# Optimization experiments

Measured on AMD Instinct MI355X. Metric: run time of the kernel, lower is better.

The kernel has to match this reference:

```python
import jax, jax.numpy as jnp
import numpy as np

N_ATOMS = 200_000
N_PAIRS = 20_000_000
N_SPECIES = 4
N_EDGES = 101  # -> 100 bins
R_MAX_GEN = 6.5  # generate some distances beyond the last edge (they are dropped)


def setup_inputs() -> dict:
    key = jax.random.key(0)
    k1, k2, k3, k4 = jax.random.split(key, 4)
    pair_dist = jax.random.uniform(k1, (N_PAIRS,), dtype=jnp.float32) * R_MAX_GEN
    pair_first = jax.random.randint(k2, (N_PAIRS,), 0, N_ATOMS)
    pair_second = jax.random.randint(k3, (N_PAIRS,), 0, N_ATOMS)
    # strict one-hot species encoding per atom (matches hippynn's one_hot input)
    species = jax.random.randint(k4, (N_ATOMS,), 0, N_SPECIES)
    one_hot = species[:, None] == jnp.arange(N_SPECIES)[None, :]
    bins = jnp.linspace(0.0, 6.0, N_EDGES).astype(jnp.float32)  # buffer from __init__
    return {
        "pair_dist": pair_dist,
        "pair_first": pair_first,
        "pair_second": pair_second,
        "one_hot": one_hot,
        "n_molecules": 512,
        "bins": bins,
    }


def reference(pair_dist, pair_first, pair_second, one_hot, n_molecules, bins):
    # Original: for each species pair (i,j), mask pairs where one_hot[pair_first,i]
    # and one_hot[pair_second,j], then histogram masked distances into `bins` via
    # broadcast-compare + diff of counts:  count in bin b = #(bins[b] <= d < bins[b+1]).
    # Fused single-pass equivalent: bucketize each pair distance and scatter-add
    # into a flat (species_i, species_j, bin) histogram.
    n_species = one_hot.shape[-1]
    n_bins = bins.shape[0] - 1

    species = jnp.argmax(one_hot, axis=-1)          # [n_atoms], one-hot -> label
    si = species[pair_first]                        # [n_pairs]
    sj = species[pair_second]                       # [n_pairs]

    # searchsorted(side='right') - 1 gives b s.t. bins[b] <= d < bins[b+1]
    b = jnp.searchsorted(bins, pair_dist, side="right") - 1
    valid = (b >= 0) & (b < n_bins)                 # drop d < bins[0] or d >= bins[-1]
    b_safe = jnp.clip(b, 0, n_bins - 1)

    flat_idx = (si * n_species + sj) * n_bins + b_safe
    weights = valid.astype(pair_dist.dtype)
    rdf = jnp.zeros((n_species * n_species * n_bins,), dtype=pair_dist.dtype)
    rdf = rdf.at[flat_idx].add(weights)
    rdf = rdf.reshape(n_species, n_species, n_bins)
    return (rdf / n_molecules)[None]                # [1, S, S, n_bins]
```

## Files before the change

kernel.cpp:

```cpp
#include <hip/hip_runtime.h>
#include <stdint.h>


#define NSPEC 4

__device__ inline int esize_from_nzw(unsigned int nzw) {
    if (nzw >= 640) return 1;
    if (nzw >= 192) return 4;
    return 8;
}

__device__ inline int get_species(const uint8_t* oh, int atom, int E) {
    if (E == 1) {
        uint32_t v = *(const uint32_t*)(oh + (size_t)atom * 4);
        if (v & 0x000000FFu) return 0;
        if (v & 0x0000FF00u) return 1;
        if (v & 0x00FF0000u) return 2;
        return 3;
    }
    const uint8_t* p = oh + (size_t)atom * 4 * E;
    for (int s = 0; s < NSPEC; ++s) {
        bool nzb = false;
        for (int b = 0; b < E; ++b) nzb |= (p[s * E + b] != 0);
        if (nzb) return s;
    }
    return 0;
}

__global__ void k_species(const uint8_t* __restrict__ oh, int n_atoms,
                          uint32_t* __restrict__ sp2,
                          unsigned int* __restrict__ counts, int n_counts) {
    __shared__ unsigned int s_nz;
    if (threadIdx.x == 0) s_nz = 0;
    __syncthreads();
    unsigned int local = 0;
    #pragma unroll
    for (int k = 0; k < 4; ++k) {
        uint32_t v = ((const uint32_t*)oh)[threadIdx.x * 4 + k];
        local += (v != 0u);
    }
    for (int off = 32; off > 0; off >>= 1) local += __shfl_down(local, off);
    if ((threadIdx.x & 63) == 0) atomicAdd(&s_nz, local);
    __syncthreads();
    const int E = esize_from_nzw(s_nz);

    const int gid = blockIdx.x * blockDim.x + threadIdx.x;
    const int gsz = gridDim.x * blockDim.x;
    for (int j = gid; j < n_counts; j += gsz) counts[j] = 0u;

    const int nw = (n_atoms + 15) >> 4;
    for (int w = gid; w < nw; w += gsz) {
        uint32_t word = 0;
        int base = w << 4;
        int lim = n_atoms - base;
        lim = lim < 16 ? lim : 16;
        for (int k = 0; k < lim; ++k)
            word |= (uint32_t)get_species(oh, base + k, E) << (k * 2);
        sp2[w] = word;
    }
}

__launch_bounds__(1024, 8) __global__
void k_hist_lds(const float* __restrict__ dist, const int* __restrict__ pf,
                const int* __restrict__ ps, const uint32_t* __restrict__ sp2,
                const float* __restrict__ bins, int n_edges, int n_words,
                int npairs, unsigned int* __restrict__ counts) {
    extern __shared__ float2 smem2[];
    const int n_bins = n_edges - 1;
    const int nh = NSPEC * NSPEC * n_bins;
    float2* eb = smem2;
    uint32_t* tab = (uint32_t*)(eb + n_bins);
    int* h = (int*)(tab + n_words);
    __shared__ int s_uniform;

    const int tid = threadIdx.x;
    if (tid == 0) s_uniform = 1;
    __syncthreads();

    for (int j = tid; j < n_words; j += blockDim.x) tab[j] = sp2[j];
    for (int j = tid; j < nh + 8; j += blockDim.x) h[j] = 0;
    const float lo = bins[0];
    const float hi = bins[n_edges - 1];
    const float w = (hi - lo) / (float)n_bins;
    for (int j = tid; j < n_bins; j += blockDim.x) {
        float2 e = make_float2(bins[j], bins[j + 1]);
        eb[j] = e;
        float id0 = lo + (float)j * w;
        float id1 = lo + (float)(j + 1) * w;
        if (fabsf(e.x - id0) > 0.25f * w || fabsf(e.y - id1) > 0.25f * w)
            atomicAnd(&s_uniform, 0);
    }
    __syncthreads();

    const float scale = (float)n_bins / (hi - lo);
    const int gid = blockIdx.x * blockDim.x + tid;
    const int gsz = gridDim.x * blockDim.x;
    const int nquads = npairs >> 2;
    const int dump = nh + (tid & 7);

    if (s_uniform) {
        for (int q = gid; q < nquads; q += gsz) {
            float4 d4 = ((const float4*)dist)[q];
            int4 f4 = ((const int4*)pf)[q];
            int4 s4 = ((const int4*)ps)[q];
            float d[4] = {d4.x, d4.y, d4.z, d4.w};
            int a0[4] = {f4.x, f4.y, f4.z, f4.w};
            int a1[4] = {s4.x, s4.y, s4.z, s4.w};
            int g[4], vld[4];
            #pragma unroll
            for (int k = 0; k < 4; ++k) {
                int gi = (int)((d[k] - lo) * scale);
                gi = gi < n_bins - 1 ? gi : n_bins - 1;
                g[k] = gi > 0 ? gi : 0;
                vld[k] = (d[k] >= lo) & (d[k] < hi);
            }
            float2 e[4];
            uint32_t wi[4], wj[4];
            #pragma unroll
            for (int k = 0; k < 4; ++k) e[k] = eb[g[k]];
            #pragma unroll
            for (int k = 0; k < 4; ++k) {
                wi[k] = tab[(unsigned)a0[k] >> 4];
                wj[k] = tab[(unsigned)a1[k] >> 4];
            }
            #pragma unroll
            for (int k = 0; k < 4; ++k) {
                int b = g[k] - (d[k] < e[k].x) + (d[k] >= e[k].y);
                int si = (int)((wi[k] >> ((a0[k] & 15) << 1)) & 3u);
                int sj = (int)((wj[k] >> ((a1[k] & 15) << 1)) & 3u);
                int idx = (si * NSPEC + sj) * n_bins + b;
                atomicAdd(&h[vld[k] ? idx : dump], 1);
            }
        }
    } else {
        for (int q = gid; q < nquads; q += gsz) {
            float4 d4 = ((const float4*)dist)[q];
            int4 f4 = ((const int4*)pf)[q];
            int4 s4 = ((const int4*)ps)[q];
            float d[4] = {d4.x, d4.y, d4.z, d4.w};
            int a0[4] = {f4.x, f4.y, f4.z, f4.w};
            int a1[4] = {s4.x, s4.y, s4.z, s4.w};
            #pragma unroll
            for (int k = 0; k < 4; ++k) {
                if (d[k] >= lo && d[k] < hi) {
                    int b = (int)((d[k] - lo) * scale);
                    b = b < n_bins - 1 ? b : n_bins - 1;
                    b = b > 0 ? b : 0;
                    while (d[k] < eb[b].x) --b;
                    while (d[k] >= eb[b].y) ++b;
                    int si = get_species((const uint8_t*)0, 0, 0);
                    (void)si;
                    int s_i = (int)((tab[(unsigned)a0[k] >> 4] >>
                                     ((a0[k] & 15) << 1)) & 3u);
                    int s_j = (int)((tab[(unsigned)a1[k] >> 4] >>
                                     ((a1[k] & 15) << 1)) & 3u);
                    atomicAdd(&h[(s_i * NSPEC + s_j) * n_bins + b], 1);
                }
            }
        }
    }
    int tail = npairs & 3;
    if (gid < tail) {
        int i = (nquads << 2) + gid;
        float d = dist[i];
        if (d >= lo && d < hi) {
            int b = (int)((d - lo) * scale);
            b = b < n_bins - 1 ? b : n_bins - 1;
            b = b > 0 ? b : 0;
            while (d < eb[b].x) --b;
            while (d >= eb[b].y) ++b;
            int a0 = pf[i], a1 = ps[i];
            int s_i = (int)((tab[(unsigned)a0 >> 4] >> ((a0 & 15) << 1)) & 3u);
            int s_j = (int)((tab[(unsigned)a1 >> 4] >> ((a1 & 15) << 1)) & 3u);
            atomicAdd(&h[(s_i * NSPEC + s_j) * n_bins + b], 1);
        }
    }

    __syncthreads();
    for (int j = tid; j < nh; j += blockDim.x) {
        int v = h[j];
        if (v) atomicAdd(&counts[j], (unsigned int)v);
    }
}

__launch_bounds__(256, 8) __global__
void k_hist_glb(const float* __restrict__ dist, const int* __restrict__ pf,
                const int* __restrict__ ps, const uint32_t* __restrict__ sp2,
                const float* __restrict__ bins, int n_edges, int npairs,
                unsigned int* __restrict__ counts) {
    const int n_bins = n_edges - 1;
    const int nh = NSPEC * NSPEC * n_bins;
    extern __shared__ float smem[];
    float* sb = smem;
    int* h = (int*)(smem + n_edges);
    const int tid = threadIdx.x;
    for (int j = tid; j < n_edges; j += blockDim.x) sb[j] = bins[j];
    for (int j = tid; j < nh; j += blockDim.x) h[j] = 0;
    __syncthreads();
    const float lo = sb[0];
    const float hi = sb[n_edges - 1];
    const float scale = (float)n_bins / (hi - lo);
    const int gid = blockIdx.x * blockDim.x + tid;
    const int gsz = gridDim.x * blockDim.x;
    auto species_of = [&](int a) -> int {
        return (int)((sp2[a >> 4] >> ((a & 15) << 1)) & 3u);
    };
    auto bin_and_add = [&](float d, int si, int sj) {
        if (d >= lo && d < hi) {
            int b = (int)((d - lo) * scale);
            b = b < n_bins - 1 ? b : n_bins - 1;
            b = b > 0 ? b : 0;
            while (d < sb[b]) --b;
            while (d >= sb[b + 1]) ++b;
            atomicAdd(&h[(si * NSPEC + sj) * n_bins + b], 1);
        }
    };
    const int nquads = npairs >> 2;
    for (int q = gid; q < nquads; q += gsz) {
        float4 d4 = ((const float4*)dist)[q];
        int4 f4 = ((const int4*)pf)[q];
        int4 s4 = ((const int4*)ps)[q];
        bin_and_add(d4.x, species_of(f4.x), species_of(s4.x));
        bin_and_add(d4.y, species_of(f4.y), species_of(s4.y));
        bin_and_add(d4.z, species_of(f4.z), species_of(s4.z));
        bin_and_add(d4.w, species_of(f4.w), species_of(s4.w));
    }
    int tail = npairs & 3;
    if (gid < tail) {
        int i = (nquads << 2) + gid;
        bin_and_add(dist[i], species_of(pf[i]), species_of(ps[i]));
    }
    __syncthreads();
    for (int j = tid; j < nh; j += blockDim.x) {
        int v = h[j];
        if (v) atomicAdd(&counts[j], (unsigned int)v);
    }
}

__global__ void k_final(const unsigned int* __restrict__ counts,
                        const int* __restrict__ nmol, float* __restrict__ out,
                        int n) {
    int i = blockIdx.x * blockDim.x + threadIdx.x;
    if (i < n) out[i] = (float)counts[i] / (float)(*nmol);
}

extern "C" void kernel_launch(void* const* d_in, const int* in_sizes, int n_in,
                              void* d_out, int out_size, void* d_ws,
                              size_t ws_size, hipStream_t stream) {
    const float* dist = (const float*)d_in[0];
    const int* pf = (const int*)d_in[1];
    const int* ps = (const int*)d_in[2];
    const uint8_t* oh = (const uint8_t*)d_in[3];
    const int* nmol = (const int*)d_in[4];
    const float* bins = (const float*)d_in[5];
    float* out = (float*)d_out;

    const int npairs = in_sizes[0];
    const int n_edges = in_sizes[5];
    const int n_bins = n_edges - 1;
    const int n_atoms = in_sizes[3] / NSPEC;
    const int nh = NSPEC * NSPEC * n_bins;

    uint8_t* ws = (uint8_t*)d_ws;
    unsigned int* counts = (unsigned int*)ws;
    uint32_t* sp2 = (uint32_t*)(ws + nh * 4 + 64);
    const int n_words = (n_atoms + 15) >> 4;

    k_species<<<256, 256, 0, stream>>>(oh, n_atoms, sp2, counts, nh);

    const size_t shmem_lds = (size_t)n_bins * 8 + (size_t)n_words * 4 +
                             (size_t)(nh + 8) * 4;
    if (shmem_lds <= 64 * 1024) {
        k_hist_lds<<<512, 1024, shmem_lds, stream>>>(
            dist, pf, ps, sp2, bins, n_edges, n_words, npairs, counts);
    } else {
        const size_t shmem = (size_t)n_edges * 4 + (size_t)nh * 4;
        k_hist_glb<<<2048, 256, shmem, stream>>>(dist, pf, ps, sp2, bins,
                                                 n_edges, npairs, counts);
    }

    k_final<<<(out_size + 255) / 256, 256, 0, stream>>>(counts, nmol, out,
                                                        out_size);
}
```

Before: 79.71 us.

## Use contiguous per-block chunks, register prefetch, and two-way privatized LDS histograms

Each block now processes a contiguous chunk of pair quads instead of a grid-strided range, and the next iteration's float4/int4 loads are issued into registers before the current quad is binned, overlapping memory latency with LDS work. The per-block histogram is split into two copies selected by wavefront parity, which is meant to reduce LDS atomic contention, and the copies are summed at flush. The cost is extra LDS (about 6.5KB more), a larger zeroing loop, and higher register pressure from the prefetch buffers. The LDS footprint stays under the 64KB threshold, so the fast path is still taken.

Measured after the change: 82.00 us. 1.03x slower.

```diff
diff --git a/kernel.cpp b/kernel.cpp
--- a/kernel.cpp
+++ b/kernel.cpp
@@ -78,7 +78,7 @@
     __syncthreads();
 
     for (int j = tid; j < n_words; j += blockDim.x) tab[j] = sp2[j];
-    for (int j = tid; j < nh + 8; j += blockDim.x) h[j] = 0;
+    for (int j = tid; j < 2 * (nh + 8); j += blockDim.x) h[j] = 0;
     const float lo = bins[0];
     const float hi = bins[n_edges - 1];
     const float w = (hi - lo) / (float)n_bins;
@@ -93,26 +93,45 @@
     __syncthreads();
 
     const float scale = (float)n_bins / (hi - lo);
-    const int gid = blockIdx.x * blockDim.x + tid;
-    const int gsz = gridDim.x * blockDim.x;
     const int nquads = npairs >> 2;
+    const int chunk = (nquads + gridDim.x - 1) / gridDim.x;
+    const int q0 = blockIdx.x * chunk;
+    const int qend = min(q0 + chunk, nquads);
+    const int qn = qend - q0;
+    const int nit = qn > 0 ? (qn + (int)blockDim.x - 1) / (int)blockDim.x : 0;
+    int* hw = h + ((tid >> 6) & 1) * (nh + 8);
     const int dump = nh + (tid & 7);
 
-    if (s_uniform) {
-        for (int q = gid; q < nquads; q += gsz) {
-            float4 d4 = ((const float4*)dist)[q];
-            int4 f4 = ((const int4*)pf)[q];
-            int4 s4 = ((const int4*)ps)[q];
-            float d[4] = {d4.x, d4.y, d4.z, d4.w};
-            int a0[4] = {f4.x, f4.y, f4.z, f4.w};
-            int a1[4] = {s4.x, s4.y, s4.z, s4.w};
+    const float4* dist4 = (const float4*)dist;
+    const int4* pf4 = (const int4*)pf;
+    const int4* ps4 = (const int4*)ps;
+
+    if (s_uniform && nit > 0) {
+        int idx = q0 + tid;
+        int lidx = min(idx, nquads - 1);
+        float4 dA = dist4[lidx];
+        int4 fA = pf4[lidx];
+        int4 sA = ps4[lidx];
+        for (int it = 0; it < nit; ++it) {
+            float4 dB;
+            int4 fB, sB;
+            if (it + 1 < nit) {
+                int nidx = min(idx + (int)blockDim.x, nquads - 1);
+                dB = dist4[nidx];
+                fB = pf4[nidx];
+                sB = ps4[nidx];
+            }
+            const int ok = idx < qend;
+            float d[4] = {dA.x, dA.y, dA.z, dA.w};
+            int a0[4] = {fA.x, fA.y, fA.z, fA.w};
+            int a1[4] = {sA.x, sA.y, sA.z, sA.w};
             int g[4], vld[4];
             #pragma unroll
             for (int k = 0; k < 4; ++k) {
                 int gi = (int)((d[k] - lo) * scale);
                 gi = gi < n_bins - 1 ? gi : n_bins - 1;
                 g[k] = gi > 0 ? gi : 0;
-                vld[k] = (d[k] >= lo) & (d[k] < hi);
+                vld[k] = ((d[k] >= lo) & (d[k] < hi)) & ok;
             }
             float2 e[4];
             uint32_t wi[4], wj[4];
@@ -128,15 +147,19 @@
                 int b = g[k] - (d[k] < e[k].x) + (d[k] >= e[k].y);
                 int si = (int)((wi[k] >> ((a0[k] & 15) << 1)) & 3u);
                 int sj = (int)((wj[k] >> ((a1[k] & 15) << 1)) & 3u);
-                int idx = (si * NSPEC + sj) * n_bins + b;
-                atomicAdd(&h[vld[k] ? idx : dump], 1);
-            }
+                int hidx = (si * NSPEC + sj) * n_bins + b;
+                atomicAdd(&hw[vld[k] ? hidx : dump], 1);
+            }
+            dA = dB;
+            fA = fB;
+            sA = sB;
+            idx += (int)blockDim.x;
         }
-    } else {
-        for (int q = gid; q < nquads; q += gsz) {
-            float4 d4 = ((const float4*)dist)[q];
-            int4 f4 = ((const int4*)pf)[q];
-            int4 s4 = ((const int4*)ps)[q];
+    } else if (nit > 0) {
+        for (int idx = q0 + tid; idx < qend; idx += (int)blockDim.x) {
+            float4 d4 = dist4[idx];
+            int4 f4 = pf4[idx];
+            int4 s4 = ps4[idx];
             float d[4] = {d4.x, d4.y, d4.z, d4.w};
             int a0[4] = {f4.x, f4.y, f4.z, f4.w};
             int a1[4] = {s4.x, s4.y, s4.z, s4.w};
@@ -148,20 +171,19 @@
                     b = b > 0 ? b : 0;
                     while (d[k] < eb[b].x) --b;
                     while (d[k] >= eb[b].y) ++b;
-                    int si = get_species((const uint8_t*)0, 0, 0);
-                    (void)si;
                     int s_i = (int)((tab[(unsigned)a0[k] >> 4] >>
                                      ((a0[k] & 15) << 1)) & 3u);
                     int s_j = (int)((tab[(unsigned)a1[k] >> 4] >>
                                      ((a1[k] & 15) << 1)) & 3u);
-                    atomicAdd(&h[(s_i * NSPEC + s_j) * n_bins + b], 1);
+                    atomicAdd(&hw[(s_i * NSPEC + s_j) * n_bins + b], 1);
                 }
             }
         }
     }
     int tail = npairs & 3;
-    if (gid < tail) {
-        int i = (nquads << 2) + gid;
+    int gtid = blockIdx.x * (int)blockDim.x + tid;
+    if (gtid < tail) {
+        int i = (nquads << 2) + gtid;
         float d = dist[i];
         if (d >= lo && d < hi) {
             int b = (int)((d - lo) * scale);
@@ -172,13 +194,13 @@
             int a0 = pf[i], a1 = ps[i];
             int s_i = (int)((tab[(unsigned)a0 >> 4] >> ((a0 & 15) << 1)) & 3u);
             int s_j = (int)((tab[(unsigned)a1 >> 4] >> ((a1 & 15) << 1)) & 3u);
-            atomicAdd(&h[(s_i * NSPEC + s_j) * n_bins + b], 1);
+            atomicAdd(&hw[(s_i * NSPEC + s_j) * n_bins + b], 1);
         }
     }
 
     __syncthreads();
     for (int j = tid; j < nh; j += blockDim.x) {
-        int v = h[j];
+        int v = h[j] + h[nh + 8 + j];
         if (v) atomicAdd(&counts[j], (unsigned int)v);
     }
 }
@@ -269,7 +291,7 @@
     k_species<<<256, 256, 0, stream>>>(oh, n_atoms, sp2, counts, nh);
 
     const size_t shmem_lds = (size_t)n_bins * 8 + (size_t)n_words * 4 +
-                             (size_t)(nh + 8) * 4;
+                             (size_t)2 * (nh + 8) * 4;
     if (shmem_lds <= 64 * 1024) {
         k_hist_lds<<<512, 1024, shmem_lds, stream>>>(
             dist, pf, ps, sp2, bins, n_edges, n_words, npairs, counts);
```

## Verify exact fast bin index at setup and replace global atomics with per-block partial reduce

Applied to the files above, without the earlier changes.

At setup, each block checks whether the scaled-index formula maps every bin edge, and the float just below it, to the correct bin. If it does, the hot loop drops the edge-table lookup and correction step. Each block also writes its LDS histogram to a per-block partial buffer, and a new reduce kernel sums those partials and normalises, replacing the global atomicAdd merge and the final kernel. This trades contended global atomics for extra workspace traffic of HIST_BLOCKS*nh words, and falls back to the old atomic path when the workspace is too small.

New measurement: 89.47 us. 12.2% more time.

```diff
diff --git a/kernel.cpp b/kernel.cpp
--- a/kernel.cpp
+++ b/kernel.cpp
@@ -3,6 +3,7 @@
 
 
 #define NSPEC 4
+#define HIST_BLOCKS 512
 
 __device__ inline int esize_from_nzw(unsigned int nzw) {
     if (nzw >= 640) return 1;
@@ -64,60 +65,69 @@
 void k_hist_lds(const float* __restrict__ dist, const int* __restrict__ pf,
                 const int* __restrict__ ps, const uint32_t* __restrict__ sp2,
                 const float* __restrict__ bins, int n_edges, int n_words,
-                int npairs, unsigned int* __restrict__ counts) {
+                int npairs, unsigned int* __restrict__ counts,
+                unsigned int* __restrict__ part) {
     extern __shared__ float2 smem2[];
     const int n_bins = n_edges - 1;
     const int nh = NSPEC * NSPEC * n_bins;
     float2* eb = smem2;
     uint32_t* tab = (uint32_t*)(eb + n_bins);
     int* h = (int*)(tab + n_words);
-    __shared__ int s_uniform;
+    __shared__ int s_exact;
 
     const int tid = threadIdx.x;
-    if (tid == 0) s_uniform = 1;
+    if (tid == 0) s_exact = 1;
     __syncthreads();
 
     for (int j = tid; j < n_words; j += blockDim.x) tab[j] = sp2[j];
     for (int j = tid; j < nh + 8; j += blockDim.x) h[j] = 0;
     const float lo = bins[0];
     const float hi = bins[n_edges - 1];
-    const float w = (hi - lo) / (float)n_bins;
-    for (int j = tid; j < n_bins; j += blockDim.x) {
-        float2 e = make_float2(bins[j], bins[j + 1]);
-        eb[j] = e;
-        float id0 = lo + (float)j * w;
-        float id1 = lo + (float)(j + 1) * w;
-        if (fabsf(e.x - id0) > 0.25f * w || fabsf(e.y - id1) > 0.25f * w)
-            atomicAnd(&s_uniform, 0);
-    }
-    __syncthreads();
-
     const float scale = (float)n_bins / (hi - lo);
+
+    for (int j = tid; j < n_edges; j += blockDim.x) {
+        float e = bins[j];
+        eb[j < n_bins ? j : 0] = make_float2(bins[j < n_bins ? j : 0],
+                                             bins[(j < n_bins ? j : 0) + 1]);
+        bool ok = true;
+        if (j < n_bins) {
+            int gi = (int)((e - lo) * scale);
+            gi = gi < n_bins - 1 ? gi : n_bins - 1;
+            gi = gi > 0 ? gi : 0;
+            ok &= (gi == j);
+        }
+        if (j >= 1) {
+            if (e <= 0.f) ok = false;
+            else {
+                float ep = __int_as_float(__float_as_int(e) - 1);
+                int gi = (int)((ep - lo) * scale);
+                gi = gi < n_bins - 1 ? gi : n_bins - 1;
+                gi = gi > 0 ? gi : 0;
+                ok &= (gi == j - 1);
+            }
+        }
+        if (!ok) atomicAnd(&s_exact, 0);
+    }
+    __syncthreads();
+
     const int gid = blockIdx.x * blockDim.x + tid;
     const int gsz = gridDim.x * blockDim.x;
     const int nquads = npairs >> 2;
     const int dump = nh + (tid & 7);
 
-    if (s_uniform) {
+    const float4* dist4 = (const float4*)dist;
+    const int4* pf4 = (const int4*)pf;
+    const int4* ps4 = (const int4*)ps;
+
+    if (s_exact) {
         for (int q = gid; q < nquads; q += gsz) {
-            float4 d4 = ((const float4*)dist)[q];
-            int4 f4 = ((const int4*)pf)[q];
-            int4 s4 = ((const int4*)ps)[q];
+            float4 d4 = dist4[q];
+            int4 f4 = pf4[q];
+            int4 s4 = ps4[q];
             float d[4] = {d4.x, d4.y, d4.z, d4.w};
             int a0[4] = {f4.x, f4.y, f4.z, f4.w};
             int a1[4] = {s4.x, s4.y, s4.z, s4.w};
-            int g[4], vld[4];
-            #pragma unroll
-            for (int k = 0; k < 4; ++k) {
-                int gi = (int)((d[k] - lo) * scale);
-                gi = gi < n_bins - 1 ? gi : n_bins - 1;
-                g[k] = gi > 0 ? gi : 0;
-                vld[k] = (d[k] >= lo) & (d[k] < hi);
-            }
-            float2 e[4];
             uint32_t wi[4], wj[4];
-            #pragma unroll
-            for (int k = 0; k < 4; ++k) e[k] = eb[g[k]];
             #pragma unroll
             for (int k = 0; k < 4; ++k) {
                 wi[k] = tab[(unsigned)a0[k] >> 4];
@@ -125,18 +135,21 @@
             }
             #pragma unroll
             for (int k = 0; k < 4; ++k) {
-                int b = g[k] - (d[k] < e[k].x) + (d[k] >= e[k].y);
+                int b = (int)((d[k] - lo) * scale);
+                b = b < n_bins - 1 ? b : n_bins - 1;
+                b = b > 0 ? b : 0;
+                int vld = (d[k] >= lo) & (d[k] < hi);
                 int si = (int)((wi[k] >> ((a0[k] & 15) << 1)) & 3u);
                 int sj = (int)((wj[k] >> ((a1[k] & 15) << 1)) & 3u);
                 int idx = (si * NSPEC + sj) * n_bins + b;
-                atomicAdd(&h[vld[k] ? idx : dump], 1);
+                atomicAdd(&h[vld ? idx : dump], 1);
             }
         }
     } else {
         for (int q = gid; q < nquads; q += gsz) {
-            float4 d4 = ((const float4*)dist)[q];
-            int4 f4 = ((const int4*)pf)[q];
-            int4 s4 = ((const int4*)ps)[q];
+            float4 d4 = dist4[q];
+            int4 f4 = pf4[q];
+            int4 s4 = ps4[q];
             float d[4] = {d4.x, d4.y, d4.z, d4.w};
             int a0[4] = {f4.x, f4.y, f4.z, f4.w};
             int a1[4] = {s4.x, s4.y, s4.z, s4.w};
@@ -148,8 +161,6 @@
                     b = b > 0 ? b : 0;
                     while (d[k] < eb[b].x) --b;
                     while (d[k] >= eb[b].y) ++b;
-                    int si = get_species((const uint8_t*)0, 0, 0);
-                    (void)si;
                     int s_i = (int)((tab[(unsigned)a0[k] >> 4] >>
                                      ((a0[k] & 15) << 1)) & 3u);
                     int s_j = (int)((tab[(unsigned)a1[k] >> 4] >>
@@ -177,9 +188,14 @@
     }
 
     __syncthreads();
-    for (int j = tid; j < nh; j += blockDim.x) {
-        int v = h[j];
-        if (v) atomicAdd(&counts[j], (unsigned int)v);
+    if (part) {
+        unsigned int* dst = part + (size_t)blockIdx.x * nh;
+        for (int j = tid; j < nh; j += blockDim.x) dst[j] = (unsigned int)h[j];
+    } else {
+        for (int j = tid; j < nh; j += blockDim.x) {
+            int v = h[j];
+            if (v) atomicAdd(&counts[j], (unsigned int)v);
+        }
     }
 }
 
@@ -237,6 +253,21 @@
     }
 }
 
+__global__ void k_reduce(const unsigned int* __restrict__ part, int nblocks,
+                         int nh, const int* __restrict__ nmol,
+                         float* __restrict__ out) {
+    const int tid = threadIdx.x;
+    const int bin = blockIdx.x * 32 + (tid >> 3);
+    const int sub = tid & 7;
+    if (bin >= nh) return;
+    unsigned int s = 0;
+    for (int k = sub; k < nblocks; k += 8) s += part[(size_t)k * nh + bin];
+    s += __shfl_down(s, 4);
+    s += __shfl_down(s, 2);
+    s += __shfl_down(s, 1);
+    if (sub == 0) out[bin] = (float)s / (float)(*nmol);
+}
+
 __global__ void k_final(const unsigned int* __restrict__ counts,
                         const int* __restrict__ nmol, float* __restrict__ out,
                         int n) {
@@ -265,20 +296,31 @@
     unsigned int* counts = (unsigned int*)ws;
     uint32_t* sp2 = (uint32_t*)(ws + nh * 4 + 64);
     const int n_words = (n_atoms + 15) >> 4;
+    size_t part_off = ((size_t)nh * 4 + 64 + (size_t)n_words * 4 + 255) &
+                      ~(size_t)255;
+    unsigned int* part = (unsigned int*)(ws + part_off);
+    const size_t need_part = part_off + (size_t)HIST_BLOCKS * nh * 4;
+    const bool use_tree = ws_size >= need_part;
 
     k_species<<<256, 256, 0, stream>>>(oh, n_atoms, sp2, counts, nh);
 
     const size_t shmem_lds = (size_t)n_bins * 8 + (size_t)n_words * 4 +
                              (size_t)(nh + 8) * 4;
     if (shmem_lds <= 64 * 1024) {
-        k_hist_lds<<<512, 1024, shmem_lds, stream>>>(
-            dist, pf, ps, sp2, bins, n_edges, n_words, npairs, counts);
+        k_hist_lds<<<HIST_BLOCKS, 1024, shmem_lds, stream>>>(
+            dist, pf, ps, sp2, bins, n_edges, n_words, npairs, counts,
+            use_tree ? part : nullptr);
     } else {
         const size_t shmem = (size_t)n_edges * 4 + (size_t)nh * 4;
         k_hist_glb<<<2048, 256, shmem, stream>>>(dist, pf, ps, sp2, bins,
                                                  n_edges, npairs, counts);
     }
 
-    k_final<<<(out_size + 255) / 256, 256, 0, stream>>>(counts, nmol, out,
-                                                        out_size);
-}
+    if (use_tree && shmem_lds <= 64 * 1024) {
+        k_reduce<<<(nh + 31) / 32, 256, 0, stream>>>(part, HIST_BLOCKS, nh,
+                                                     nmol, out);
+    } else {
+        k_final<<<(out_size + 255) / 256, 256, 0, stream>>>(counts, nmol, out,
+                                                            out_size);
+    }
+}
```
